# Kernel optimization log

Hardware: AMD Instinct MI355X
Metric: run time of the kernel (lower is better)

Reference implementation:

```python
import jax, jax.numpy as jnp
import numpy as np

B = 128          # number of trees (batched identical perfect-binary structure)
LEAVES = 1024    # leaves per tree -> N = 2*LEAVES - 1 = 2047 nodes, heap order
D_IN = 512       # input_size
NL = 64          # num_labels


def setup_inputs() -> dict:
    key = jax.random.key(0)
    k1, k2, k3, k4 = jax.random.split(key, 4)
    N = 2 * LEAVES - 1
    hidden = jax.random.normal(k1, (B, N, D_IN), dtype=jnp.float32)
    W = jax.random.normal(k2, (D_IN, NL), dtype=jnp.float32) / np.sqrt(D_IN)
    b = jax.random.normal(k3, (NL,), dtype=jnp.float32) * 0.02
    trans = jax.random.normal(k4, (NL, NL), dtype=jnp.float32) / np.sqrt(NL)
    return {"hidden": hidden, "W": W, "b": b, "trans": trans}


def reference(hidden, W, b, trans):
    # hidden: [B, N, D] with N = 2^depth - 1 nodes in heap (level) order:
    # node i's children are 2i+1, 2i+2; level d occupies [2^d-1, 2^{d+1}-1).
    Bn, N, D = hidden.shape
    L = trans.shape[0]
    depth = int(np.log2(N + 1))  # number of levels

    # emission scores for every node at once (single_h_pred, no dense layer)
    emis = jnp.einsum('bnd,dl->bnl', hidden, W) + b  # [B, N, L]

    # leaves level
    n = 2 ** (depth - 1)
    inside = emis[:, n - 1: n - 1 + n]  # [B, n, L]

    # inside algorithm, bottom-up:
    # inside[p, a] = emis[p, a]
    #             + logsumexp_l(inside_left[l]  + trans[a, l])
    #             + logsumexp_r(inside_right[r] + trans[a, r])
    for d in range(depth - 2, -1, -1):
        n = 2 ** d
        left = inside[:, 0::2]   # [B, n, L]
        right = inside[:, 1::2]  # [B, n, L]
        lt = jax.nn.logsumexp(left[:, :, None, :] + trans[None, None, :, :], axis=-1)
        rt = jax.nn.logsumexp(right[:, :, None, :] + trans[None, None, :, :], axis=-1)
        inside = emis[:, n - 1: n - 1 + n] + lt + rt  # [B, n, L]

    return inside[:, 0]  # root inside scores, [B, L]
```

## Files before the change

kernel.cpp:

```cpp
#include <hip/hip_runtime.h>
#include <math.h>

#define B_      128
#define NNODES  2047
#define NL_     64
#define DIN     512

__global__ __launch_bounds__(256) void kexp_trans(const float* __restrict__ trans,
                                                  float* __restrict__ E) {
    int i = blockIdx.x * 256 + threadIdx.x;
    if (i < NL_ * NL_) E[i] = __expf(trans[i]);
}

__global__ __launch_bounds__(256) void kgemm(const float* __restrict__ H,
                                             const float* __restrict__ W,
                                             const float* __restrict__ bias,
                                             float* __restrict__ emis) {
    __shared__ float As[64][68];
    __shared__ float Bs[64][64];
    int t  = threadIdx.x;
    int rowBase = blockIdx.x * 64;
    int tx = t & 15;
    int ty = t >> 4;
    float acc[4][4] = {};

    for (int kc = 0; kc < DIN; kc += 64) {
        __syncthreads();
        #pragma unroll
        for (int p = 0; p < 4; ++p) {
            int f = t + p * 256;
            int r = f >> 4, q = f & 15;
            float4 av = *(const float4*)(H + (rowBase + r) * DIN + kc + q * 4);
            *(float4*)&As[r][q * 4] = av;
            float4 wv = *(const float4*)(W + (kc + r) * NL_ + q * 4);
            *(float4*)&Bs[r][q * 4] = wv;
        }
        __syncthreads();
        #pragma unroll
        for (int k = 0; k < 64; ++k) {
            float a0 = As[ty * 4 + 0][k];
            float a1 = As[ty * 4 + 1][k];
            float a2 = As[ty * 4 + 2][k];
            float a3 = As[ty * 4 + 3][k];
            float4 bv = *(const float4*)&Bs[k][tx * 4];
            acc[0][0] = fmaf(a0, bv.x, acc[0][0]); acc[0][1] = fmaf(a0, bv.y, acc[0][1]);
            acc[0][2] = fmaf(a0, bv.z, acc[0][2]); acc[0][3] = fmaf(a0, bv.w, acc[0][3]);
            acc[1][0] = fmaf(a1, bv.x, acc[1][0]); acc[1][1] = fmaf(a1, bv.y, acc[1][1]);
            acc[1][2] = fmaf(a1, bv.z, acc[1][2]); acc[1][3] = fmaf(a1, bv.w, acc[1][3]);
            acc[2][0] = fmaf(a2, bv.x, acc[2][0]); acc[2][1] = fmaf(a2, bv.y, acc[2][1]);
            acc[2][2] = fmaf(a2, bv.z, acc[2][2]); acc[2][3] = fmaf(a2, bv.w, acc[2][3]);
            acc[3][0] = fmaf(a3, bv.x, acc[3][0]); acc[3][1] = fmaf(a3, bv.y, acc[3][1]);
            acc[3][2] = fmaf(a3, bv.z, acc[3][2]); acc[3][3] = fmaf(a3, bv.w, acc[3][3]);
        }
    }
    float4 bv = *(const float4*)(bias + tx * 4);
    #pragma unroll
    for (int i = 0; i < 4; ++i) {
        float4 o;
        o.x = acc[i][0] + bv.x; o.y = acc[i][1] + bv.y;
        o.z = acc[i][2] + bv.z; o.w = acc[i][3] + bv.w;
        *(float4*)(emis + (rowBase + ty * 4 + i) * NL_ + tx * 4) = o;
    }
}

__global__ __launch_bounds__(64) void klevel(float* __restrict__ inside,
                                             const float* __restrict__ E,
                                             int d) {
    int lane   = threadIdx.x;
    int n      = 1 << d;
    int groups = (B_ << d) >> 6;
    int J      = 1024 / groups;
    int jw     = 64 / J;
    int tg     = blockIdx.x / J;
    int j0     = (blockIdx.x % J) * jw;

    int task = tg * 64 + lane;
    int b    = task >> d;
    int i    = task & (n - 1);
    int g    = n - 1 + i;
    int rowL = (b * NNODES + 2 * g + 1) << 6;
    int rowG = (b * NNODES + g) << 6;

    float el[64], er[64];
    const float4* pC = (const float4*)(inside + rowL);
    #pragma unroll
    for (int q = 0; q < 16; ++q) {
        float4 v = pC[q];
        el[4*q] = v.x; el[4*q+1] = v.y; el[4*q+2] = v.z; el[4*q+3] = v.w;
    }
    #pragma unroll
    for (int q = 0; q < 16; ++q) {
        float4 v = pC[16 + q];
        er[4*q] = v.x; er[4*q+1] = v.y; er[4*q+2] = v.z; er[4*q+3] = v.w;
    }
    float ml = el[0], mr = er[0];
    #pragma unroll
    for (int k = 1; k < 64; ++k) { ml = fmaxf(ml, el[k]); mr = fmaxf(mr, er[k]); }
    #pragma unroll
    for (int k = 0; k < 64; ++k) {
        el[k] = __expf(el[k] - ml);
        er[k] = __expf(er[k] - mr);
    }
    float mbase = ml + mr;

    for (int jj = 0; jj < jw; ++jj) {
        int j = j0 + jj;
        const float4* Er = (const float4*)(E + (j << 6));
        float accl = 0.f, accr = 0.f;
        #pragma unroll
        for (int q = 0; q < 16; ++q) {
            float4 e = Er[q];
            accl = fmaf(el[4*q+0], e.x, accl); accl = fmaf(el[4*q+1], e.y, accl);
            accl = fmaf(el[4*q+2], e.z, accl); accl = fmaf(el[4*q+3], e.w, accl);
            accr = fmaf(er[4*q+0], e.x, accr); accr = fmaf(er[4*q+1], e.y, accr);
            accr = fmaf(er[4*q+2], e.z, accr); accr = fmaf(er[4*q+3], e.w, accr);
        }
        float ev = inside[rowG + j];
        inside[rowG + j] = ev + mbase + __logf(accl) + __logf(accr);
    }
}

__global__ __launch_bounds__(256) void ktail(float* __restrict__ inside,
                                             const float* __restrict__ E,
                                             float* __restrict__ out) {
    int b    = blockIdx.x;
    int lane = threadIdx.x & 63;
    int wid  = threadIdx.x >> 6;

    float Ereg[64];
    const float4* E4 = (const float4*)(E + lane * NL_);
    #pragma unroll
    for (int q = 0; q < 16; ++q) {
        float4 v = E4[q];
        Ereg[4*q] = v.x; Ereg[4*q+1] = v.y; Ereg[4*q+2] = v.z; Ereg[4*q+3] = v.w;
    }
    int base = b * NNODES;

    for (int d = 5; d >= 0; --d) {
        int n = 1 << d;
        for (int i = wid; i < n; i += 4) {
            int g    = n - 1 + i;
            int rowC = (base + 2 * g + 1) << 6;
            float lf = inside[rowC + lane];
            float rf = inside[rowC + 64 + lane];
            float ml = lf, mr = rf;
            #pragma unroll
            for (int s = 32; s >= 1; s >>= 1) {
                ml = fmaxf(ml, __shfl_xor(ml, s));
                mr = fmaxf(mr, __shfl_xor(mr, s));
            }
            float el = __expf(lf - ml);
            float er = __expf(rf - mr);
            float accl = 0.f, accr = 0.f;
            #pragma unroll
            for (int k = 0; k < 64; ++k) {
                float ek = __int_as_float(__builtin_amdgcn_readlane(__float_as_int(el), k));
                float rk = __int_as_float(__builtin_amdgcn_readlane(__float_as_int(er), k));
                accl = fmaf(ek, Ereg[k], accl);
                accr = fmaf(rk, Ereg[k], accr);
            }
            int rowG  = (base + g) << 6;
            float res = inside[rowG + lane] + ml + mr + __logf(accl) + __logf(accr);
            if (d == 0) out[b * NL_ + lane] = res;
            else        inside[rowG + lane] = res;
        }
        __syncthreads();
    }
}

extern "C" void kernel_launch(void* const* d_in, const int* in_sizes, int n_in,
                              void* d_out, int out_size, void* d_ws, size_t ws_size,
                              hipStream_t stream) {
    const float* hidden = (const float*)d_in[0];
    const float* W      = (const float*)d_in[1];
    const float* bias   = (const float*)d_in[2];
    const float* trans  = (const float*)d_in[3];
    float* out    = (float*)d_out;
    float* E      = (float*)d_ws;
    float* inside = E + NL_ * NL_;

    kexp_trans<<<16, 256, 0, stream>>>(trans, E);
    kgemm<<<(B_ * NNODES) / 64, 256, 0, stream>>>(hidden, W, bias, inside);
    for (int d = 9; d >= 6; --d)
        klevel<<<1024, 64, 0, stream>>>(inside, E, d);
    ktail<<<B_, 256, 0, stream>>>(inside, E, out);
}
```

Measured before the change: 944.3 us.

## Use bf16 MFMA for emission GEMM and widen level kernel grid

The emission GEMM now converts hidden rows to bf16 while staging them in shared memory and multiplies with a pre-transposed bf16 copy of W using 16x16x32 MFMA instructions, instead of scalar fp32 FMAs. A new prep kernel builds the transposed bf16 W in workspace. The level kernel launches twice as many blocks, each covering fewer output labels, and writes results as float4 in groups of four. The change trades emission precision (bf16 inputs) for matrix-core throughput, while the kernel still reads the large fp32 hidden tensor from memory.

```diff
diff --git a/kernel.cpp b/kernel.cpp
--- a/kernel.cpp
+++ b/kernel.cpp
@@ -6,70 +6,98 @@
 #define NL_     64
 #define DIN     512
 
+typedef __attribute__((ext_vector_type(8))) short short8;
+typedef __attribute__((ext_vector_type(4))) float v4f;
+
+static __device__ inline unsigned short f2bf(float x) {
+    unsigned u = __float_as_uint(x);
+    u = (u + 0x7FFFu + ((u >> 16) & 1u)) >> 16;
+    return (unsigned short)u;
+}
+
 __global__ __launch_bounds__(256) void kexp_trans(const float* __restrict__ trans,
                                                   float* __restrict__ E) {
     int i = blockIdx.x * 256 + threadIdx.x;
     if (i < NL_ * NL_) E[i] = __expf(trans[i]);
 }
 
+__global__ __launch_bounds__(256) void kprep(const float* __restrict__ W,
+                                             unsigned short* __restrict__ Wt) {
+    int i = blockIdx.x * 256 + threadIdx.x;
+    int k = i >> 6, n = i & 63;
+    Wt[n * DIN + k] = f2bf(W[i]);
+}
+
 __global__ __launch_bounds__(256) void kgemm(const float* __restrict__ H,
-                                             const float* __restrict__ W,
+                                             const unsigned short* __restrict__ Wt,
                                              const float* __restrict__ bias,
                                              float* __restrict__ emis) {
-    __shared__ float As[64][68];
-    __shared__ float Bs[64][64];
-    int t  = threadIdx.x;
+    __shared__ unsigned short Al[64 * 72];
+    __shared__ unsigned short Wl[64 * 72];
+    int t = threadIdx.x;
     int rowBase = blockIdx.x * 64;
-    int tx = t & 15;
-    int ty = t >> 4;
-    float acc[4][4] = {};
+    int lane = t & 63;
+    int w    = t >> 6;
+    int ln   = lane & 15;
+    int quad = lane >> 4;
+
+    v4f acc[4];
+    #pragma unroll
+    for (int i = 0; i < 4; ++i) acc[i] = (v4f){0.f, 0.f, 0.f, 0.f};
+
+    int r   = t >> 2;
+    int sub = t & 3;
+    const float* hrow = H + (long)(rowBase + r) * DIN + sub * 16;
+    const unsigned short* wrow = Wt + r * DIN + sub * 8;
 
     for (int kc = 0; kc < DIN; kc += 64) {
         __syncthreads();
         #pragma unroll
-        for (int p = 0; p < 4; ++p) {
-            int f = t + p * 256;
-            int r = f >> 4, q = f & 15;
-            float4 av = *(const float4*)(H + (rowBase + r) * DIN + kc + q * 4);
-            *(float4*)&As[r][q * 4] = av;
-            float4 wv = *(const float4*)(W + (kc + r) * NL_ + q * 4);
-            *(float4*)&Bs[r][q * 4] = wv;
+        for (int i = 0; i < 4; ++i) {
+            float4 v = *(const float4*)(hrow + kc + i * 4);
+            unsigned long long pk =
+                (unsigned long long)f2bf(v.x)
+              | ((unsigned long long)f2bf(v.y) << 16)
+              | ((unsigned long long)f2bf(v.z) << 32)
+              | ((unsigned long long)f2bf(v.w) << 48);
+            *(unsigned long long*)&Al[r * 72 + sub * 16 + i * 4] = pk;
+        }
+        #pragma unroll
+        for (int i = 0; i < 2; ++i) {
+            uint4 wv = *(const uint4*)(wrow + kc + i * 32);
+            *(uint4*)&Wl[r * 72 + sub * 8 + i * 32] = wv;
         }
         __syncthreads();
-        #pragma unroll
-        for (int k = 0; k < 64; ++k) {
-            float a0 = As[ty * 4 + 0][k];
-            float a1 = As[ty * 4 + 1][k];
-            float a2 = As[ty * 4 + 2][k];
-            float a3 = As[ty * 4 + 3][k];
-            float4 bv = *(const float4*)&Bs[k][tx * 4];
-            acc[0][0] = fmaf(a0, bv.x, acc[0][0]); acc[0][1] = fmaf(a0, bv.y, acc[0][1]);
-            acc[0][2] = fmaf(a0, bv.z, acc[0][2]); acc[0][3] = fmaf(a0, bv.w, acc[0][3]);
-            acc[1][0] = fmaf(a1, bv.x, acc[1][0]); acc[1][1] = fmaf(a1, bv.y, acc[1][1]);
-            acc[1][2] = fmaf(a1, bv.z, acc[1][2]); acc[1][3] = fmaf(a1, bv.w, acc[1][3]);
-            acc[2][0] = fmaf(a2, bv.x, acc[2][0]); acc[2][1] = fmaf(a2, bv.y, acc[2][1]);
-            acc[2][2] = fmaf(a2, bv.z, acc[2][2]); acc[2][3] = fmaf(a2, bv.w, acc[2][3]);
-            acc[3][0] = fmaf(a3, bv.x, acc[3][0]); acc[3][1] = fmaf(a3, bv.y, acc[3][1]);
-            acc[3][2] = fmaf(a3, bv.z, acc[3][2]); acc[3][3] = fmaf(a3, bv.w, acc[3][3]);
-        }
-    }
-    float4 bv = *(const float4*)(bias + tx * 4);
-    #pragma unroll
-    for (int i = 0; i < 4; ++i) {
-        float4 o;
-        o.x = acc[i][0] + bv.x; o.y = acc[i][1] + bv.y;
-        o.z = acc[i][2] + bv.z; o.w = acc[i][3] + bv.w;
-        *(float4*)(emis + (rowBase + ty * 4 + i) * NL_ + tx * 4) = o;
-    }
-}
-
-__global__ __launch_bounds__(64) void klevel(float* __restrict__ inside,
-                                             const float* __restrict__ E,
-                                             int d) {
+        const unsigned short* Ab = &Al[(w * 16 + ln) * 72];
+        const unsigned short* Wb = &Wl[ln * 72];
+        #pragma unroll
+        for (int ks = 0; ks < 2; ++ks) {
+            short8 af = *(const short8*)(Ab + ks * 32 + quad * 8);
+            #pragma unroll
+            for (int nt = 0; nt < 4; ++nt) {
+                short8 bf = *(const short8*)(Wb + nt * 16 * 72 + ks * 32 + quad * 8);
+                acc[nt] = __builtin_amdgcn_mfma_f32_16x16x32_bf16(af, bf, acc[nt], 0, 0, 0);
+            }
+        }
+    }
+    #pragma unroll
+    for (int nt = 0; nt < 4; ++nt) {
+        float bv = bias[nt * 16 + ln];
+        #pragma unroll
+        for (int rg = 0; rg < 4; ++rg) {
+            int row = rowBase + w * 16 + quad * 4 + rg;
+            emis[(long)row * NL_ + nt * 16 + ln] = acc[nt][rg] + bv;
+        }
+    }
+}
+
+__global__ __launch_bounds__(64, 2) void klevel(float* __restrict__ inside,
+                                                const float* __restrict__ E,
+                                                int d) {
     int lane   = threadIdx.x;
     int n      = 1 << d;
     int groups = (B_ << d) >> 6;
-    int J      = 1024 / groups;
+    int J      = 2048 / groups;
     int jw     = 64 / J;
     int tg     = blockIdx.x / J;
     int j0     = (blockIdx.x % J) * jw;
@@ -103,20 +131,26 @@
     }
     float mbase = ml + mr;
 
-    for (int jj = 0; jj < jw; ++jj) {
-        int j = j0 + jj;
-        const float4* Er = (const float4*)(E + (j << 6));
-        float accl = 0.f, accr = 0.f;
-        #pragma unroll
-        for (int q = 0; q < 16; ++q) {
-            float4 e = Er[q];
-            accl = fmaf(el[4*q+0], e.x, accl); accl = fmaf(el[4*q+1], e.y, accl);
-            accl = fmaf(el[4*q+2], e.z, accl); accl = fmaf(el[4*q+3], e.w, accl);
-            accr = fmaf(er[4*q+0], e.x, accr); accr = fmaf(er[4*q+1], e.y, accr);
-            accr = fmaf(er[4*q+2], e.z, accr); accr = fmaf(er[4*q+3], e.w, accr);
-        }
-        float ev = inside[rowG + j];
-        inside[rowG + j] = ev + mbase + __logf(accl) + __logf(accr);
+    for (int j4 = 0; j4 < jw; j4 += 4) {
+        float res[4];
+        #pragma unroll
+        for (int jj = 0; jj < 4; ++jj) {
+            const float4* Er = (const float4*)(E + ((j0 + j4 + jj) << 6));
+            float accl = 0.f, accr = 0.f;
+            #pragma unroll
+            for (int q = 0; q < 16; ++q) {
+                float4 e = Er[q];
+                accl = fmaf(el[4*q+0], e.x, accl); accl = fmaf(el[4*q+1], e.y, accl);
+                accl = fmaf(el[4*q+2], e.z, accl); accl = fmaf(el[4*q+3], e.w, accl);
+                accr = fmaf(er[4*q+0], e.x, accr); accr = fmaf(er[4*q+1], e.y, accr);
+                accr = fmaf(er[4*q+2], e.z, accr); accr = fmaf(er[4*q+3], e.w, accr);
+            }
+            res[jj] = mbase + __logf(accl) + __logf(accr);
+        }
+        float4* pg = (float4*)(inside + rowG + j0 + j4);
+        float4 ev = *pg;
+        ev.x += res[0]; ev.y += res[1]; ev.z += res[2]; ev.w += res[3];
+        *pg = ev;
     }
 }
 
@@ -175,13 +209,15 @@
     const float* W      = (const float*)d_in[1];
     const float* bias   = (const float*)d_in[2];
     const float* trans  = (const float*)d_in[3];
-    float* out    = (float*)d_out;
-    float* E      = (float*)d_ws;
-    float* inside = E + NL_ * NL_;
+    float* out = (float*)d_out;
+    float* E   = (float*)d_ws;
+    unsigned short* Wt = (unsigned short*)(E + NL_ * NL_);
+    float* inside = E + NL_ * NL_ + (DIN * NL_ / 2);
 
     kexp_trans<<<16, 256, 0, stream>>>(trans, E);
-    kgemm<<<(B_ * NNODES) / 64, 256, 0, stream>>>(hidden, W, bias, inside);
+    kprep<<<(DIN * NL_) / 256, 256, 0, stream>>>(W, Wt);
+    kgemm<<<(B_ * NNODES) / 64, 256, 0, stream>>>(hidden, Wt, bias, inside);
     for (int d = 9; d >= 6; --d)
-        klevel<<<1024, 64, 0, stream>>>(inside, E, d);
+        klevel<<<2048, 64, 0, stream>>>(inside, E, d);
     ktail<<<B_, 256, 0, stream>>>(inside, E, out);
 }
```

After: 824.8 us. 1.14x faster.
